# Kernel optimization log

Measured on AMD Instinct MI355X. Metric: run time of the kernel, lower is better.

## Reference

```python
import math
import jax, jax.numpy as jnp
import numpy as np


def get_slopes(n):
    def pow2(n):
        start = 2.0 ** (-(2.0 ** (-(math.log2(n) - 3))))
        return [start * (start ** i) for i in range(n)]
    if math.log2(n).is_integer():
        return pow2(n)
    c = 2 ** math.floor(math.log2(n))
    return pow2(c) + get_slopes(2 * c)[0::2][: n - c]


def setup_inputs() -> dict:
    key = jax.random.key(0)
    B, T, C = 2, 2048, 1024
    ks = jax.random.split(key, 9)
    std = 0.02
    n_layers = 12
    inp = {
        "x": jax.random.normal(ks[0], (B, T, C), dtype=jnp.float32),
        # weights stored as [in, out] (transpose of torch Linear.weight)
        "Wq": std * jax.random.normal(ks[1], (C, C), dtype=jnp.float32),
        "bq": jnp.zeros((C,), dtype=jnp.float32),
        "Wk": std * jax.random.normal(ks[2], (C, C), dtype=jnp.float32),
        "bk": jnp.zeros((C,), dtype=jnp.float32),
        "Wv": std * jax.random.normal(ks[3], (C, C), dtype=jnp.float32),
        "bv": jnp.zeros((C,), dtype=jnp.float32),
        # fc_resid gets std 0.02/sqrt(2*num_layers)
        "Wo": (std / math.sqrt(2 * n_layers)) * jax.random.normal(ks[4], (C, C), dtype=jnp.float32),
        "bo": jnp.zeros((C,), dtype=jnp.float32),
        "n_head": 16,
    }
    return inp


def reference(x, Wq, bq, Wk, bk, Wv, bv, Wo, bo, n_head):
    B, T, C = x.shape
    hd = C // n_head
    # QKV projections, split heads: [B, nh, T, hd]
    def proj(W, b):
        return (x @ W + b).reshape(B, T, n_head, hd).transpose(0, 2, 1, 3)
    q, k, v = proj(Wq, bq), proj(Wk, bk), proj(Wv, bv)

    # ALiBi bias: bias[h, i, j] = -slope_h * (i - j) for j <= i, -inf above diag
    slopes = jnp.asarray(get_slopes(n_head), dtype=x.dtype)  # [nh]
    idx = jnp.arange(T)
    dist = (idx[:, None] - idx[None, :]).astype(x.dtype)  # [T, T], i - j
    bias = -slopes[:, None, None] * dist  # [nh, T, T]
    causal = idx[:, None] >= idx[None, :]
    bias = jnp.where(causal[None], bias, jnp.asarray(-jnp.inf, dtype=x.dtype))

    scale = 1.0 / math.sqrt(hd)
    scores = jnp.einsum("bnqh,bnkh->bnqk", q, k) * scale + bias[None]
    att = jax.nn.softmax(scores, axis=-1)
    y = jnp.einsum("bnqk,bnkh->bnqh", att, v)  # [B, nh, T, hd]
    y = y.transpose(0, 2, 1, 3).reshape(B, T, C)
    return y @ Wo + bo
```

## Files before the change

### kernel.cpp

```cpp
#include <hip/hip_runtime.h>


typedef unsigned short u16;
typedef unsigned int u32;
typedef __attribute__((ext_vector_type(8))) short bf16x8;
typedef __attribute__((ext_vector_type(4))) float f32x4;
typedef __attribute__((ext_vector_type(4))) unsigned short u16x4;

#define MFMA16x16(A, B, C_) __builtin_amdgcn_mfma_f32_16x16x32_bf16((A), (B), (C_), 0, 0, 0)

__device__ __forceinline__ u16 f2bf(float f) {
  u32 x = __builtin_bit_cast(u32, f);
  x += 0x7fff + ((x >> 16) & 1);
  return (u16)(x >> 16);
}

__device__ __forceinline__ void gload_lds16(const u16* g, u16* l) {
  __builtin_amdgcn_global_load_lds(
      (const __attribute__((address_space(1))) void*)g,
      (__attribute__((address_space(3))) void*)l, 16, 0, 0);
}

constexpr int T = 2048, C = 1024, HD = 64;
constexpr int BT = 2 * T;

__device__ __forceinline__ bf16x8 ldsfrag(const u16* lds, int row, int kchunk) {
  return *(const bf16x8*)(lds + row * 64 + (((kchunk) ^ (row & 7)) << 3));
}

__global__ __launch_bounds__(256) void prep_kernel(
    const float* __restrict__ xin, u16* __restrict__ xc,
    const float* __restrict__ w0, const float* __restrict__ w1,
    const float* __restrict__ w2, const float* __restrict__ w3,
    u16* __restrict__ wqkvT, u16* __restrict__ woT) {
  __shared__ u16 tile[32][33];
  const int bz = blockIdx.x, tid = threadIdx.x;
  if (bz < 2048) {
    int i = (bz * 256 + tid) * 8;
    const float4 a = *(const float4*)(xin + i);
    const float4 b = *(const float4*)(xin + i + 4);
    uint4 o;
    o.x = (u32)f2bf(a.x) | ((u32)f2bf(a.y) << 16);
    o.y = (u32)f2bf(a.z) | ((u32)f2bf(a.w) << 16);
    o.z = (u32)f2bf(b.x) | ((u32)f2bf(b.y) << 16);
    o.w = (u32)f2bf(b.z) | ((u32)f2bf(b.w) << 16);
    *(uint4*)(xc + i) = o;
    return;
  }
  const int t = bz - 2048;
  const int z = t >> 10, rem = t & 1023;
  const int bx = rem & 31, by = rem >> 5;
  const float* in = (z == 0) ? w0 : (z == 1) ? w1 : (z == 2) ? w2 : w3;
  u16* out = (z < 3) ? (wqkvT + (size_t)z * (1u << 20)) : woT;
  const int tx = tid & 31, ty = tid >> 5;
  int x = bx * 32 + tx;
#pragma unroll
  for (int i = 0; i < 4; i++) {
    int y = by * 32 + ty + i * 8;
    tile[ty + i * 8][tx] = f2bf(in[y * 1024 + x]);
  }
  __syncthreads();
  int xo = by * 32 + tx;
#pragma unroll
  for (int i = 0; i < 4; i++) {
    int yo = bx * 32 + ty + i * 8;
    out[yo * 1024 + xo] = tile[tx][ty + i * 8];
  }
}

__global__ __launch_bounds__(512, 2) void gemm_qkv_kernel(
    const u16* __restrict__ A, const u16* __restrict__ Bt,
    const float* __restrict__ b0, const float* __restrict__ b1,
    const float* __restrict__ b2,
    u16* __restrict__ qout, u16* __restrict__ kout, u16* __restrict__ vtout) {
  constexpr int K = 1024, BK = 32, NT = K / BK;
  __shared__ __align__(16) u16 ring[4][2][256 * BK];

  const int tid = threadIdx.x;
  const int w = tid >> 6, lane = tid & 63;
  const int l15 = lane & 15, quad = lane >> 4;
  const int wr = w >> 2, wc = w & 3;
  const int bid = blockIdx.y * 12 + blockIdx.x;
  const int swz = (bid & 7) * 24 + (bid >> 3);
  const int m0 = (swz / 12) * 256, n0 = (swz % 12) * 256;
  const int rw = lane >> 2;
  const int pc = lane & 3;

  const u16* Ag = A + (size_t)m0 * K;
  const u16* Bg = Bt + (size_t)n0 * K;

  f32x4 acc[8][4] = {};

  auto STAGE = [&](int kt, int s) {
#pragma unroll
    for (int j = 0; j < 2; j++) {
      int row = j * 128 + w * 16 + rw;
      int cl = pc ^ (row & 3);
      gload_lds16(Ag + (size_t)row * K + kt * BK + cl * 8,
                  &ring[s][0][(j * 128 + w * 16) * BK]);
      gload_lds16(Bg + (size_t)row * K + kt * BK + cl * 8,
                  &ring[s][1][(j * 128 + w * 16) * BK]);
    }
  };

  STAGE(0, 0); STAGE(1, 1); STAGE(2, 2);
  asm volatile("s_waitcnt vmcnt(8)" ::: "memory");
  __builtin_amdgcn_s_barrier();

#pragma unroll 1
  for (int t = 0; t < NT; ++t) {
    const int s = t & 3;
    if (t + 3 < NT) STAGE(t + 3, (t + 3) & 3);

    const u16* As = ring[s][0];
    const u16* Bs = ring[s][1];
    bf16x8 bfr[4], afr[8];
#pragma unroll
    for (int ni = 0; ni < 4; ni++) {
      int row = wc * 64 + ni * 16 + l15;
      bfr[ni] = *(const bf16x8*)(Bs + row * BK + ((quad ^ (row & 3)) << 3));
    }
#pragma unroll
    for (int mi = 0; mi < 8; mi++) {
      int row = wr * 128 + mi * 16 + l15;
      afr[mi] = *(const bf16x8*)(As + row * BK + ((quad ^ (row & 3)) << 3));
    }
    __builtin_amdgcn_s_setprio(1);
#pragma unroll
    for (int mi = 0; mi < 8; mi++)
#pragma unroll
      for (int ni = 0; ni < 4; ni++)
        acc[mi][ni] = MFMA16x16(afr[mi], bfr[ni], acc[mi][ni]);
    __builtin_amdgcn_s_setprio(0);

    if (t + 3 < NT)
      asm volatile("s_waitcnt vmcnt(8)" ::: "memory");
    else if (t + 2 < NT)
      asm volatile("s_waitcnt vmcnt(4)" ::: "memory");
    else if (t + 1 < NT)
      asm volatile("s_waitcnt vmcnt(0)" ::: "memory");
    if (t + 1 < NT) __builtin_amdgcn_s_barrier();
  }

  const int sel = n0 >> 10;
  const int nloc = n0 & 1023;
  if (sel < 2) {
    u16* D = (sel == 0) ? qout : kout;
    const float* bias = (sel == 0) ? b0 : b1;
#pragma unroll
    for (int mi = 0; mi < 8; mi++)
#pragma unroll
      for (int ni = 0; ni < 4; ni++) {
        int rb = m0 + wr * 128 + mi * 16 + quad * 4;
        int col = nloc + wc * 64 + ni * 16 + l15;
        float bb = bias[col];
#pragma unroll
        for (int r = 0; r < 4; r++)
          D[(size_t)(rb + r) * 1024 + col] = f2bf(acc[mi][ni][r] + bb);
      }
  } else {
#pragma unroll
    for (int mi = 0; mi < 8; mi++)
#pragma unroll
      for (int ni = 0; ni < 4; ni++) {
        int rb = m0 + wr * 128 + mi * 16 + quad * 4;
        int c = nloc + wc * 64 + ni * 16 + l15;
        float bb = b2[c];
        u16x4 pk;
#pragma unroll
        for (int r = 0; r < 4; r++) pk[r] = f2bf(acc[mi][ni][r] + bb);
        *(u16x4*)(vtout + (size_t)c * 4096 + rb) = pk;
      }
  }
}

__global__ __launch_bounds__(256, 2) void gemm_out_kernel(
    const u16* __restrict__ A, const u16* __restrict__ Bt,
    const float* __restrict__ bias, float* __restrict__ fout) {
  constexpr int K = 1024, BK = 32, NT = K / BK;
  __shared__ __align__(16) u16 ring[4][2][128 * BK];

  const int tid = threadIdx.x;
  const int w = tid >> 6, lane = tid & 63;
  const int l15 = lane & 15, quad = lane >> 4;
  const int wr = w >> 1, wc = w & 1;
  const int bid = blockIdx.y * 8 + blockIdx.x;
  const int swz = (bid & 7) * 32 + (bid >> 3);
  const int m0 = (swz >> 3) * 128, n0 = (swz & 7) * 128;
  const int rw = lane >> 2;
  const int pc = lane & 3;

  const u16* Ag = A + (size_t)m0 * K;
  const u16* Bg = Bt + (size_t)n0 * K;

  f32x4 acc[4][4] = {};

  auto STAGE = [&](int kt, int s) {
#pragma unroll
    for (int j = 0; j < 2; j++) {
      int row = j * 64 + w * 16 + rw;
      int cl = pc ^ (row & 3);
      gload_lds16(Ag + (size_t)row * K + kt * BK + cl * 8,
                  &ring[s][0][(j * 64 + w * 16) * BK]);
      gload_lds16(Bg + (size_t)row * K + kt * BK + cl * 8,
                  &ring[s][1][(j * 64 + w * 16) * BK]);
    }
  };

  STAGE(0, 0); STAGE(1, 1); STAGE(2, 2);
  asm volatile("s_waitcnt vmcnt(8)" ::: "memory");
  __builtin_amdgcn_s_barrier();

#pragma unroll 1
  for (int t = 0; t < NT; ++t) {
    const int s = t & 3;
    if (t + 3 < NT) STAGE(t + 3, (t + 3) & 3);

    const u16* As = ring[s][0];
    const u16* Bs = ring[s][1];
    bf16x8 bfr[4], afr[4];
#pragma unroll
    for (int ni = 0; ni < 4; ni++) {
      int row = wc * 64 + ni * 16 + l15;
      bfr[ni] = *(const bf16x8*)(Bs + row * BK + ((quad ^ (row & 3)) << 3));
    }
#pragma unroll
    for (int mi = 0; mi < 4; mi++) {
      int row = wr * 64 + mi * 16 + l15;
      afr[mi] = *(const bf16x8*)(As + row * BK + ((quad ^ (row & 3)) << 3));
    }
    __builtin_amdgcn_s_setprio(1);
#pragma unroll
    for (int mi = 0; mi < 4; mi++)
#pragma unroll
      for (int ni = 0; ni < 4; ni++)
        acc[mi][ni] = MFMA16x16(afr[mi], bfr[ni], acc[mi][ni]);
    __builtin_amdgcn_s_setprio(0);

    if (t + 3 < NT)
      asm volatile("s_waitcnt vmcnt(8)" ::: "memory");
    else if (t + 2 < NT)
      asm volatile("s_waitcnt vmcnt(4)" ::: "memory");
    else if (t + 1 < NT)
      asm volatile("s_waitcnt vmcnt(0)" ::: "memory");
    if (t + 1 < NT) __builtin_amdgcn_s_barrier();
  }

#pragma unroll
  for (int mi = 0; mi < 4; mi++)
#pragma unroll
    for (int ni = 0; ni < 4; ni++) {
      int rb = m0 + wr * 64 + mi * 16 + quad * 4;
      int col = n0 + wc * 64 + ni * 16 + l15;
      float bb = bias[col];
#pragma unroll
      for (int r = 0; r < 4; r++)
        fout[(size_t)(rb + r) * 1024 + col] = acc[mi][ni][r] + bb;
    }
}

__global__ __launch_bounds__(512, 4) void attn_kernel(
    const u16* __restrict__ qbuf, const u16* __restrict__ kbuf,
    const u16* __restrict__ vtbuf, u16* __restrict__ ybuf) {
  __shared__ __align__(16) u16 KVs[4][64 * 64];
  __shared__ __align__(16) u16 Ps[8][16 * 64];

  const int tid = threadIdx.x;
  const int w = tid >> 6, lane = tid & 63;
  const int wq = w & 3, g = w >> 2;
  const int l15 = lane & 15, quad = lane >> 4;
  const int bh = blockIdx.y, b = bh >> 4, h = bh & 15;
  const float slope = exp2f(-0.5f * (float)(h + 1));
  const float slope128 = slope * 128.f;
  const int gsub = (lane & 7) ^ ((lane >> 3) & 7);
  const int rsub = lane >> 3;

  const u16* kbase0 = kbuf + (size_t)b * T * C + h * HD;
  const u16* vtbase0 = vtbuf + (size_t)h * HD * BT + (size_t)b * T;
  u16* Pw = Ps[w];
  const int st = w >> 1;
  const int skind = st & 1;
  const int sjt = st >> 1;
  const int srb = (w & 1) * 32;

#pragma unroll 1
  for (int half = 0; half < 2; half++) {
    const int qt = half == 0 ? (31 - (int)blockIdx.x) : (int)blockIdx.x;

    const u16* qb = qbuf + (size_t)(b * T + qt * 64 + wq * 16 + l15) * C + h * HD;
    bf16x8 aq0 = *(const bf16x8*)(qb + quad * 8);
    bf16x8 aq1 = *(const bf16x8*)(qb + 32 + quad * 8);

    f32x4 o[4] = {};
    float lsum[4] = {0.f, 0.f, 0.f, 0.f};
    float br[4][4];
    const int ig0 = qt * 64 + wq * 16 + quad * 4;
#pragma unroll
    for (int ni = 0; ni < 4; ni++)
#pragma unroll
      for (int r = 0; r < 4; r++)
        br[ni][r] = slope * (float)(g * 64 + ni * 16 + l15 - ig0 - r);

    const int iters = (qt + 2) >> 1;
#pragma unroll 1
    for (int it = 0; it < iters; it++) {
      __syncthreads();
      {
        int jtv = 2 * it + sjt;
        int jtr = jtv > qt ? qt : jtv;
        const u16* base = skind ? (vtbase0 + jtr * 64)
                                : (kbase0 + (size_t)jtr * 64 * C);
        const int stride = skind ? BT : C;
        u16* dst = KVs[skind * 2 + sjt] + srb * 64;
#pragma unroll
        for (int c2 = 0; c2 < 4; c2++)
          gload_lds16(base + (size_t)(srb + c2 * 8 + rsub) * stride + gsub * 8,
                      dst + c2 * 8 * 64);
      }
      __syncthreads();

      const int jtv = 2 * it + g;
      const u16* Kw = KVs[g];
      const u16* Vw = KVs[2 + g];

      f32x4 s[4];
#pragma unroll
      for (int ni = 0; ni < 4; ni++) {
        bf16x8 kf0 = ldsfrag(Kw, ni * 16 + l15, quad);
        bf16x8 kf1 = ldsfrag(Kw, ni * 16 + l15, 4 + quad);
        f32x4 z = {0.f, 0.f, 0.f, 0.f};
        z = MFMA16x16(aq0, kf0, z);
        z = MFMA16x16(aq1, kf1, z);
        s[ni] = z;
      }

      const bool edge = (jtv >= qt);
#pragma unroll
      for (int ni = 0; ni < 4; ni++)
#pragma unroll
        for (int r = 0; r < 4; r++) {
          float p = __expf(fmaf(s[ni][r], 0.125f, br[ni][r]));
          if (edge && (jtv * 64 + ni * 16 + l15) > (ig0 + r)) p = 0.f;
          lsum[r] += p;
          int prow = quad * 4 + r, pcol = ni * 16 + l15;
          Pw[prow * 64 + (((pcol >> 3) ^ (prow & 7)) << 3) + (pcol & 7)] = f2bf(p);
          br[ni][r] += slope128;
        }

      bf16x8 pa0 = ldsfrag(Pw, l15, quad);
      bf16x8 pa1 = ldsfrag(Pw, l15, 4 + quad);
#pragma unroll
      for (int ni = 0; ni < 4; ni++) {
        bf16x8 vf0 = ldsfrag(Vw, ni * 16 + l15, quad);
        bf16x8 vf1 = ldsfrag(Vw, ni * 16 + l15, 4 + quad);
        o[ni] = MFMA16x16(pa0, vf0, o[ni]);
        o[ni] = MFMA16x16(pa1, vf1, o[ni]);
      }
    }

    __syncthreads();
    float* sc = (float*)KVs;
    float* Osc = sc + wq * 1024;
    float* Lsc = sc + 4096 + wq * 256;
    if (g == 1) {
#pragma unroll
      for (int ni = 0; ni < 4; ni++)
#pragma unroll
        for (int r = 0; r < 4; r++)
          Osc[(quad * 4 + r) * 64 + ni * 16 + l15] = o[ni][r];
#pragma unroll
      for (int r = 0; r < 4; r++)
        Lsc[(quad * 4 + r) * 16 + l15] = lsum[r];
    }
    __syncthreads();
    if (g == 0) {
#pragma unroll
      for (int ni = 0; ni < 4; ni++)
#pragma unroll
        for (int r = 0; r < 4; r++)
          o[ni][r] += Osc[(quad * 4 + r) * 64 + ni * 16 + l15];
#pragma unroll
      for (int r = 0; r < 4; r++) {
        float l = lsum[r] + Lsc[(quad * 4 + r) * 16 + l15];
        l += __shfl_xor(l, 1);
        l += __shfl_xor(l, 2);
        l += __shfl_xor(l, 4);
        l += __shfl_xor(l, 8);
        float inv = 1.f / l;
        int row_g = b * T + qt * 64 + wq * 16 + quad * 4 + r;
        u16* yrow = ybuf + (size_t)row_g * C + h * HD;
#pragma unroll
        for (int ni = 0; ni < 4; ni++)
          yrow[ni * 16 + l15] = f2bf(o[ni][r] * inv);
      }
    }
  }
}

extern "C" void kernel_launch(void* const* d_in, const int* in_sizes, int n_in,
                              void* d_out, int out_size, void* d_ws, size_t ws_size,
                              hipStream_t stream) {
  (void)in_sizes; (void)n_in; (void)out_size; (void)ws_size;
  const float* x  = (const float*)d_in[0];
  const float* Wq = (const float*)d_in[1];
  const float* bq = (const float*)d_in[2];
  const float* Wk = (const float*)d_in[3];
  const float* bk = (const float*)d_in[4];
  const float* Wv = (const float*)d_in[5];
  const float* bv = (const float*)d_in[6];
  const float* Wo = (const float*)d_in[7];
  const float* bo = (const float*)d_in[8];

  u16* ws = (u16*)d_ws;
  constexpr size_t M1 = 1u << 20;
  u16* wqkvT = ws;
  u16* woT   = ws + 3 * M1;
  u16* xc    = ws + 4 * M1;
  u16* qbuf  = ws + 8 * M1;
  u16* vtbuf = ws + 12 * M1;
  u16* kbuf  = (u16*)d_out;
  u16* ybuf  = qbuf;

  prep_kernel<<<6144, 256, 0, stream>>>(x, xc, Wq, Wk, Wv, Wo, wqkvT, woT);
  gemm_qkv_kernel<<<dim3(12, 16), 512, 0, stream>>>(
      xc, wqkvT, bq, bk, bv, qbuf, kbuf, vtbuf);
  attn_kernel<<<dim3(16, 32), 512, 0, stream>>>(qbuf, kbuf, vtbuf, ybuf);
  gemm_out_kernel<<<dim3(8, 32), 256, 0, stream>>>(ybuf, woT, bo, (float*)d_out);
}
```

Baseline: 196.3 us.

## Give each attention wave 32 query rows to reuse K/V fragments across two tiles

The attention kernel now uses 4 waves (256 threads) instead of 8. Each wave handles 32 query rows as two 16-row sub-tiles that share the same K and V LDS fragment loads, and each wave issues all 8 K/V tile load chunks itself. The softmax switches from __expf to exp2f with the log2(e) factor folded into the scale and the ALiBi slope. This halves LDS fragment reads per MFMA and cuts the wave count, at the cost of more registers per wave, lower launch-bound occupancy and more serialized global-to-LDS load work per wave.

```diff
diff --git a/kernel.cpp b/kernel.cpp
--- a/kernel.cpp
+++ b/kernel.cpp
@@ -259,47 +259,52 @@
     }
 }
 
-__global__ __launch_bounds__(512, 4) void attn_kernel(
+__global__ __launch_bounds__(256, 3) void attn_kernel(
     const u16* __restrict__ qbuf, const u16* __restrict__ kbuf,
     const u16* __restrict__ vtbuf, u16* __restrict__ ybuf) {
   __shared__ __align__(16) u16 KVs[4][64 * 64];
-  __shared__ __align__(16) u16 Ps[8][16 * 64];
+  __shared__ __align__(16) u16 Ps[4][32 * 64];
 
   const int tid = threadIdx.x;
   const int w = tid >> 6, lane = tid & 63;
-  const int wq = w & 3, g = w >> 2;
+  const int wq = w & 1, g = w >> 1;
   const int l15 = lane & 15, quad = lane >> 4;
   const int bh = blockIdx.y, b = bh >> 4, h = bh & 15;
-  const float slope = exp2f(-0.5f * (float)(h + 1));
-  const float slope128 = slope * 128.f;
+  constexpr float LOG2E = 1.44269504f;
+  constexpr float SC = 0.125f * LOG2E;
+  const float slope2 = exp2f(-0.5f * (float)(h + 1)) * LOG2E;
+  const float slope128 = slope2 * 128.f;
+  const float s16 = slope2 * 16.f;
   const int gsub = (lane & 7) ^ ((lane >> 3) & 7);
   const int rsub = lane >> 3;
 
   const u16* kbase0 = kbuf + (size_t)b * T * C + h * HD;
   const u16* vtbase0 = vtbuf + (size_t)h * HD * BT + (size_t)b * T;
   u16* Pw = Ps[w];
-  const int st = w >> 1;
-  const int skind = st & 1;
-  const int sjt = st >> 1;
-  const int srb = (w & 1) * 32;
+  const int skind = w >> 1;
+  const int sjt = w & 1;
 
 #pragma unroll 1
   for (int half = 0; half < 2; half++) {
     const int qt = half == 0 ? (31 - (int)blockIdx.x) : (int)blockIdx.x;
 
-    const u16* qb = qbuf + (size_t)(b * T + qt * 64 + wq * 16 + l15) * C + h * HD;
-    bf16x8 aq0 = *(const bf16x8*)(qb + quad * 8);
-    bf16x8 aq1 = *(const bf16x8*)(qb + 32 + quad * 8);
-
-    f32x4 o[4] = {};
-    float lsum[4] = {0.f, 0.f, 0.f, 0.f};
+    const u16* qb0 = qbuf + (size_t)(b * T + qt * 64 + wq * 32 + l15) * C + h * HD;
+    const u16* qb1 = qb0 + (size_t)16 * C;
+    bf16x8 aq00 = *(const bf16x8*)(qb0 + quad * 8);
+    bf16x8 aq01 = *(const bf16x8*)(qb0 + 32 + quad * 8);
+    bf16x8 aq10 = *(const bf16x8*)(qb1 + quad * 8);
+    bf16x8 aq11 = *(const bf16x8*)(qb1 + 32 + quad * 8);
+
+    f32x4 o0[4] = {}, o1[4] = {};
+    float lsum0[4] = {0.f, 0.f, 0.f, 0.f};
+    float lsum1[4] = {0.f, 0.f, 0.f, 0.f};
     float br[4][4];
-    const int ig0 = qt * 64 + wq * 16 + quad * 4;
+    const int ig0 = qt * 64 + wq * 32 + quad * 4;
 #pragma unroll
     for (int ni = 0; ni < 4; ni++)
 #pragma unroll
       for (int r = 0; r < 4; r++)
-        br[ni][r] = slope * (float)(g * 64 + ni * 16 + l15 - ig0 - r);
+        br[ni][r] = slope2 * (float)(g * 64 + ni * 16 + l15 - ig0 - r);
 
     const int iters = (qt + 2) >> 1;
 #pragma unroll 1
@@ -311,10 +316,10 @@
         const u16* base = skind ? (vtbase0 + jtr * 64)
                                 : (kbase0 + (size_t)jtr * 64 * C);
         const int stride = skind ? BT : C;
-        u16* dst = KVs[skind * 2 + sjt] + srb * 64;
-#pragma unroll
-        for (int c2 = 0; c2 < 4; c2++)
-          gload_lds16(base + (size_t)(srb + c2 * 8 + rsub) * stride + gsub * 8,
+        u16* dst = KVs[w];
+#pragma unroll
+        for (int c2 = 0; c2 < 8; c2++)
+          gload_lds16(base + (size_t)(c2 * 8 + rsub) * stride + gsub * 8,
                       dst + c2 * 8 * 64);
       }
       __syncthreads();
@@ -323,15 +328,18 @@
       const u16* Kw = KVs[g];
       const u16* Vw = KVs[2 + g];
 
-      f32x4 s[4];
+      f32x4 s0[4], s1[4];
 #pragma unroll
       for (int ni = 0; ni < 4; ni++) {
         bf16x8 kf0 = ldsfrag(Kw, ni * 16 + l15, quad);
         bf16x8 kf1 = ldsfrag(Kw, ni * 16 + l15, 4 + quad);
-        f32x4 z = {0.f, 0.f, 0.f, 0.f};
-        z = MFMA16x16(aq0, kf0, z);
-        z = MFMA16x16(aq1, kf1, z);
-        s[ni] = z;
+        f32x4 z0 = {0.f, 0.f, 0.f, 0.f};
+        f32x4 z1 = {0.f, 0.f, 0.f, 0.f};
+        z0 = MFMA16x16(aq00, kf0, z0);
+        z0 = MFMA16x16(aq01, kf1, z0);
+        z1 = MFMA16x16(aq10, kf0, z1);
+        z1 = MFMA16x16(aq11, kf1, z1);
+        s0[ni] = z0; s1[ni] = z1;
       }
 
       const bool edge = (jtv >= qt);
@@ -339,59 +347,86 @@
       for (int ni = 0; ni < 4; ni++)
 #pragma unroll
         for (int r = 0; r < 4; r++) {
-          float p = __expf(fmaf(s[ni][r], 0.125f, br[ni][r]));
-          if (edge && (jtv * 64 + ni * 16 + l15) > (ig0 + r)) p = 0.f;
-          lsum[r] += p;
-          int prow = quad * 4 + r, pcol = ni * 16 + l15;
-          Pw[prow * 64 + (((pcol >> 3) ^ (prow & 7)) << 3) + (pcol & 7)] = f2bf(p);
+          const int jj = jtv * 64 + ni * 16 + l15;
+          float p0 = exp2f(fmaf(s0[ni][r], SC, br[ni][r]));
+          float p1 = exp2f(fmaf(s1[ni][r], SC, br[ni][r]) - s16);
+          if (edge) {
+            if (jj > ig0 + r) p0 = 0.f;
+            if (jj > ig0 + 16 + r) p1 = 0.f;
+          }
+          lsum0[r] += p0;
+          lsum1[r] += p1;
+          const int pcol = ni * 16 + l15;
+          const int prow0 = quad * 4 + r;
+          const int po = (((pcol >> 3) ^ (prow0 & 7)) << 3) + (pcol & 7);
+          Pw[prow0 * 64 + po] = f2bf(p0);
+          Pw[(prow0 + 16) * 64 + po] = f2bf(p1);
           br[ni][r] += slope128;
         }
 
-      bf16x8 pa0 = ldsfrag(Pw, l15, quad);
-      bf16x8 pa1 = ldsfrag(Pw, l15, 4 + quad);
+      bf16x8 pa00 = ldsfrag(Pw, l15, quad);
+      bf16x8 pa01 = ldsfrag(Pw, l15, 4 + quad);
+      bf16x8 pa10 = ldsfrag(Pw, 16 + l15, quad);
+      bf16x8 pa11 = ldsfrag(Pw, 16 + l15, 4 + quad);
 #pragma unroll
       for (int ni = 0; ni < 4; ni++) {
         bf16x8 vf0 = ldsfrag(Vw, ni * 16 + l15, quad);
         bf16x8 vf1 = ldsfrag(Vw, ni * 16 + l15, 4 + quad);
-        o[ni] = MFMA16x16(pa0, vf0, o[ni]);
-        o[ni] = MFMA16x16(pa1, vf1, o[ni]);
+        o0[ni] = MFMA16x16(pa00, vf0, o0[ni]);
+        o0[ni] = MFMA16x16(pa01, vf1, o0[ni]);
+        o1[ni] = MFMA16x16(pa10, vf0, o1[ni]);
+        o1[ni] = MFMA16x16(pa11, vf1, o1[ni]);
       }
     }
 
     __syncthreads();
     float* sc = (float*)KVs;
-    float* Osc = sc + wq * 1024;
-    float* Lsc = sc + 4096 + wq * 256;
+    float* Osc = sc + wq * 2048;
+    float* Lsc = sc + 4096 + wq * 512;
     if (g == 1) {
 #pragma unroll
       for (int ni = 0; ni < 4; ni++)
 #pragma unroll
-        for (int r = 0; r < 4; r++)
-          Osc[(quad * 4 + r) * 64 + ni * 16 + l15] = o[ni][r];
-#pragma unroll
-      for (int r = 0; r < 4; r++)
-        Lsc[(quad * 4 + r) * 16 + l15] = lsum[r];
+        for (int r = 0; r < 4; r++) {
+          Osc[(quad * 4 + r) * 64 + ni * 16 + l15] = o0[ni][r];
+          Osc[(16 + quad * 4 + r) * 64 + ni * 16 + l15] = o1[ni][r];
+        }
+#pragma unroll
+      for (int r = 0; r < 4; r++) {
+        Lsc[(quad * 4 + r) * 16 + l15] = lsum0[r];
+        Lsc[(16 + quad * 4 + r) * 16 + l15] = lsum1[r];
+      }
     }
     __syncthreads();
     if (g == 0) {
 #pragma unroll
       for (int ni = 0; ni < 4; ni++)
 #pragma unroll
-        for (int r = 0; r < 4; r++)
-          o[ni][r] += Osc[(quad * 4 + r) * 64 + ni * 16 + l15];
+        for (int r = 0; r < 4; r++) {
+          o0[ni][r] += Osc[(quad * 4 + r) * 64 + ni * 16 + l15];
+          o1[ni][r] += Osc[(16 + quad * 4 + r) * 64 + ni * 16 + l15];
+        }
 #pragma unroll
       for (int r = 0; r < 4; r++) {
-        float l = lsum[r] + Lsc[(quad * 4 + r) * 16 + l15];
-        l += __shfl_xor(l, 1);
-        l += __shfl_xor(l, 2);
-        l += __shfl_xor(l, 4);
-        l += __shfl_xor(l, 8);
-        float inv = 1.f / l;
-        int row_g = b * T + qt * 64 + wq * 16 + quad * 4 + r;
-        u16* yrow = ybuf + (size_t)row_g * C + h * HD;
-#pragma unroll
-        for (int ni = 0; ni < 4; ni++)
-          yrow[ni * 16 + l15] = f2bf(o[ni][r] * inv);
+        float l0 = lsum0[r] + Lsc[(quad * 4 + r) * 16 + l15];
+        float l1 = lsum1[r] + Lsc[(16 + quad * 4 + r) * 16 + l15];
+        l0 += __shfl_xor(l0, 1);
+        l0 += __shfl_xor(l0, 2);
+        l0 += __shfl_xor(l0, 4);
+        l0 += __shfl_xor(l0, 8);
+        l1 += __shfl_xor(l1, 1);
+        l1 += __shfl_xor(l1, 2);
+        l1 += __shfl_xor(l1, 4);
+        l1 += __shfl_xor(l1, 8);
+        float inv0 = 1.f / l0, inv1 = 1.f / l1;
+        int row0 = b * T + qt * 64 + wq * 32 + quad * 4 + r;
+        u16* y0 = ybuf + (size_t)row0 * C + h * HD;
+        u16* y1 = y0 + (size_t)16 * C;
+#pragma unroll
+        for (int ni = 0; ni < 4; ni++) {
+          y0[ni * 16 + l15] = f2bf(o0[ni][r] * inv0);
+          y1[ni * 16 + l15] = f2bf(o1[ni][r] * inv1);
+        }
       }
     }
   }
@@ -424,6 +459,6 @@
   prep_kernel<<<6144, 256, 0, stream>>>(x, xc, Wq, Wk, Wv, Wo, wqkvT, woT);
   gemm_qkv_kernel<<<dim3(12, 16), 512, 0, stream>>>(
       xc, wqkvT, bq, bk, bv, qbuf, kbuf, vtbuf);
-  attn_kernel<<<dim3(16, 32), 512, 0, stream>>>(qbuf, kbuf, vtbuf, ybuf);
+  attn_kernel<<<dim3(16, 32), 256, 0, stream>>>(qbuf, kbuf, vtbuf, ybuf);
   gemm_out_kernel<<<dim3(8, 32), 256, 0, stream>>>(ybuf, woT, bo, (float*)d_out);
 }
```

Result: slower. 216.0 us (+10.1%).
